# Kernel tuning notes

Measured on AMD Instinct MI355X. Metric: run time of the kernel, lower is better.

## Reference

```python
import jax, jax.numpy as jnp
import numpy as np

N = 50000
E = 800000
IN_DIM = 128
HID = 64
HEADS = 4
OUT_DIM = 121
NEG_SLOPE = 0.2
EPS = 1e-16


def setup_inputs() -> dict:
    key = jax.random.key(0)
    ks = jax.random.split(key, 16)
    glorot = lambda k, shape: jax.random.normal(k, shape, jnp.float32) * (2.0 / (shape[0] + shape[-1])) ** 0.5
    HC = HEADS * HID
    return {
        "x": jax.random.normal(ks[0], (N, IN_DIM), jnp.float32),
        "edge_index": jax.random.randint(ks[1], (2, E), 0, N, jnp.int64),
        # conv1: GATConv(IN_DIM -> HID, heads=HEADS, concat)
        "W1": glorot(ks[2], (IN_DIM, HC)),
        "att_src1": glorot(ks[3], (HEADS, HID)),
        "att_dst1": glorot(ks[4], (HEADS, HID)),
        "b1": jnp.zeros((HC,), jnp.float32),
        # conv2: GATConv(HC -> HID, heads=HEADS, concat)
        "W2": glorot(ks[5], (HC, HC)),
        "att_src2": glorot(ks[6], (HEADS, HID)),
        "att_dst2": glorot(ks[7], (HEADS, HID)),
        "b2": jnp.zeros((HC,), jnp.float32),
        # post_mp: Linear(HC, HID) -> Dropout -> Linear(HID, OUT_DIM)
        "Wm1": glorot(ks[8], (HC, HID)),
        "bm1": jnp.zeros((HID,), jnp.float32),
        "Wm2": glorot(ks[9], (HID, OUT_DIM)),
        "bm2": jnp.zeros((OUT_DIM,), jnp.float32),
    }


def gat_conv(x, src, dst, W, att_src, att_dst, b):
    """PyG GATConv (concat=True, add_self_loops already applied to src/dst)."""
    n = x.shape[0]
    h = (x @ W).reshape(n, HEADS, -1)                     # [N, H, C]
    a_s = jnp.einsum("nhc,hc->nh", h, att_src)            # [N, H]
    a_d = jnp.einsum("nhc,hc->nh", h, att_dst)            # [N, H]
    e = jax.nn.leaky_relu(a_s[src] + a_d[dst], NEG_SLOPE)  # [Etot, H]
    # segment softmax over destination nodes
    m = jax.ops.segment_max(e, dst, num_segments=n)       # [N, H]
    ex = jnp.exp(e - m[dst])
    denom = jax.ops.segment_sum(ex, dst, num_segments=n)  # [N, H]
    alpha = ex / (denom[dst] + EPS)                        # [Etot, H]
    out = jax.ops.segment_sum(alpha[:, :, None] * h[src], dst, num_segments=n)  # [N, H, C]
    return out.reshape(n, -1) + b


def reference(x, edge_index, W1, att_src1, att_dst1, b1, W2, att_src2, att_dst2, b2, Wm1, bm1, Wm2, bm2):
    n = x.shape[0]
    loops = jnp.arange(n, dtype=edge_index.dtype)
    src = jnp.concatenate([edge_index[0], loops])
    dst = jnp.concatenate([edge_index[1], loops])
    h = jax.nn.relu(gat_conv(x, src, dst, W1, att_src1, att_dst1, b1))
    h = jax.nn.relu(gat_conv(h, src, dst, W2, att_src2, att_dst2, b2))
    h = h @ Wm1 + bm1
    h = h @ Wm2 + bm2
    return jax.nn.sigmoid(h)
```

## Files before the change

### kernel.cpp

```cpp
#include <hip/hip_runtime.h>
#include <hip/hip_bf16.h>
#include <float.h>

#define HEADS 4
#define HID 64
#define HC 256
#define NEG_SLOPE 0.2f
#define EPS 1e-16f

typedef short bf16x8 __attribute__((ext_vector_type(8)));
typedef float f32x4 __attribute__((ext_vector_type(4)));
typedef unsigned short ushort8 __attribute__((ext_vector_type(8)));

__device__ __forceinline__ float bflo(unsigned u) { return __uint_as_float(u << 16); }
__device__ __forceinline__ float bfhi(unsigned u) { return __uint_as_float(u & 0xffff0000u); }
__device__ __forceinline__ unsigned packbf2(float a, float b) {
  __hip_bfloat16 ha = __float2bfloat16(a), hb = __float2bfloat16(b);
  unsigned short ua = *reinterpret_cast<unsigned short*>(&ha);
  unsigned short ub = *reinterpret_cast<unsigned short*>(&hb);
  return (unsigned)ua | ((unsigned)ub << 16);
}

#define PK 40

__global__ void __launch_bounds__(256) conv_gemm_attn(
    const __hip_bfloat16* __restrict__ A, const __hip_bfloat16* __restrict__ Bt,
    __hip_bfloat16* __restrict__ Cb,
    const float* __restrict__ att_s, const float* __restrict__ att_d,
    float* __restrict__ a_s, float* __restrict__ a_d,
    float* __restrict__ blockmax, int M, int K) {
  __shared__ unsigned short As[2][64 * PK];
  __shared__ unsigned short Bs[2][256 * PK];
  int tid = threadIdx.x;
  int lane = tid & 63, w = tid >> 6;
  int col16 = lane & 15, quad = lane >> 4;
  int row0 = blockIdx.x * 64;
  const unsigned short* Ag = (const unsigned short*)A;
  const unsigned short* Bg = (const unsigned short*)Bt;

  int ar = tid >> 2;
  int ako = (tid & 3) << 3;
  int agr = row0 + ar; if (agr >= M) agr = M - 1;
  const unsigned short* aga = Ag + (size_t)agr * K + ako;

  f32x4 acc[4][4] = {};
  int niter = K >> 5;

  ushort8 pa, pb[4];
  pa = *(const ushort8*)(aga);
#pragma unroll
  for (int p = 0; p < 4; p++) {
    int i2 = tid + (p << 8);
    int br = i2 >> 2, bko = (i2 & 3) << 3;
    pb[p] = *(const ushort8*)(Bg + (size_t)br * K + bko);
  }
  *(ushort8*)(&As[0][ar * PK + ako]) = pa;
#pragma unroll
  for (int p = 0; p < 4; p++) {
    int i2 = tid + (p << 8);
    int br = i2 >> 2, bko = (i2 & 3) << 3;
    *(ushort8*)(&Bs[0][br * PK + bko]) = pb[p];
  }
  __syncthreads();

  for (int it = 0; it < niter; ++it) {
    int cur = it & 1, nxt = cur ^ 1;
    int k1 = (it + 1) << 5;
    if (it + 1 < niter) {
      pa = *(const ushort8*)(aga + k1);
#pragma unroll
      for (int p = 0; p < 4; p++) {
        int i2 = tid + (p << 8);
        int br = i2 >> 2, bko = (i2 & 3) << 3;
        pb[p] = *(const ushort8*)(Bg + (size_t)br * K + k1 + bko);
      }
    }
    bf16x8 a[4], b[4];
#pragma unroll
    for (int i = 0; i < 4; i++)
      a[i] = *(const bf16x8*)(&As[cur][(i * 16 + col16) * PK + quad * 8]);
#pragma unroll
    for (int j = 0; j < 4; j++)
      b[j] = *(const bf16x8*)(&Bs[cur][((w << 6) + j * 16 + col16) * PK + quad * 8]);
#pragma unroll
    for (int i = 0; i < 4; i++)
#pragma unroll
      for (int j = 0; j < 4; j++)
        acc[i][j] = __builtin_amdgcn_mfma_f32_16x16x32_bf16(a[i], b[j], acc[i][j], 0, 0, 0);
    if (it + 1 < niter) {
      *(ushort8*)(&As[nxt][ar * PK + ako]) = pa;
#pragma unroll
      for (int p = 0; p < 4; p++) {
        int i2 = tid + (p << 8);
        int br = i2 >> 2, bko = (i2 & 3) << 3;
        *(ushort8*)(&Bs[nxt][br * PK + bko]) = pb[p];
      }
    }
    __syncthreads();
  }

#pragma unroll
  for (int i = 0; i < 4; i++) {
#pragma unroll
    for (int j = 0; j < 4; j++) {
      int gc = (w << 6) + j * 16 + col16;
      int grb = row0 + i * 16 + quad * 4;
#pragma unroll
      for (int r = 0; r < 4; r++) {
        int gr = grb + r;
        if (gr < M) Cb[(size_t)gr * 256 + gc] = __float2bfloat16(acc[i][j][r]);
      }
    }
  }

  float ws4[4], wd4[4];
#pragma unroll
  for (int j = 0; j < 4; j++) {
    ws4[j] = att_s[(w << 6) + j * 16 + col16];
    wd4[j] = att_d[(w << 6) + j * 16 + col16];
  }
  float wavemax = -FLT_MAX;
#pragma unroll
  for (int i = 0; i < 4; i++) {
#pragma unroll
    for (int r = 0; r < 4; r++) {
      float vs = 0.f, vd = 0.f;
#pragma unroll
      for (int j = 0; j < 4; j++) {
        vs += acc[i][j][r] * ws4[j];
        vd += acc[i][j][r] * wd4[j];
      }
#pragma unroll
      for (int off = 1; off < 16; off <<= 1) {
        vs += __shfl_xor(vs, off);
        vd += __shfl_xor(vd, off);
      }
      int gr = row0 + i * 16 + quad * 4 + r;
      if (col16 == 0 && gr < M) {
        a_s[(size_t)gr * 4 + w] = vs;
        a_d[(size_t)gr * 4 + w] = vd;
      }
      wavemax = fmaxf(wavemax, vs);
    }
  }
  wavemax = fmaxf(wavemax, __shfl_xor(wavemax, 16));
  wavemax = fmaxf(wavemax, __shfl_xor(wavemax, 32));
  if (lane == 0) blockmax[(size_t)blockIdx.x * 4 + w] = wavemax;
}

__global__ void __launch_bounds__(256) reduce_gmax(const float* __restrict__ blockmax,
                                                   float* __restrict__ gmaxf, int goff, int nb) {
  __shared__ float wm[4][4];
  int tid = threadIdx.x, lane = tid & 63, w = tid >> 6;
  int hd = tid & 3;
  float m = -FLT_MAX;
  for (int i = tid >> 2; i < nb; i += 64)
    m = fmaxf(m, blockmax[(size_t)i * 4 + hd]);
#pragma unroll
  for (int off = 4; off < 64; off <<= 1)
    m = fmaxf(m, __shfl_xor(m, off));
  if (lane < 4) wm[w][lane] = m;
  __syncthreads();
  if (tid < 4) {
    float r = fmaxf(fmaxf(wm[0][tid], wm[1][tid]), fmaxf(wm[2][tid], wm[3][tid]));
    gmaxf[goff + tid] = r;
  }
}

#define TS 72

__global__ void __launch_bounds__(256) postmp_fused(
    const __hip_bfloat16* __restrict__ A, const __hip_bfloat16* __restrict__ Wm1t,
    const __hip_bfloat16* __restrict__ Wm2t, const float* __restrict__ bm1,
    const float* __restrict__ bm2, float* __restrict__ out, int M) {
  __shared__ unsigned short As[128 * PK];
  __shared__ unsigned short Bs[64 * PK];
  __shared__ unsigned short T[128 * TS];
  __shared__ unsigned short W2s[128 * TS];
  int tid = threadIdx.x;
  int lane = tid & 63, w = tid >> 6;
  int col16 = lane & 15, quad = lane >> 4;
  int row0 = blockIdx.x * 128;
  const unsigned short* Ag = (const unsigned short*)A;
  const unsigned short* Bg = (const unsigned short*)Wm1t;
  const unsigned short* W2g = (const unsigned short*)Wm2t;

#pragma unroll
  for (int c = tid; c < 1024; c += 256) {
    int r = c >> 3, ko = (c & 7) << 3;
    ushort8 v = {};
    if (r < 121) v = *(const ushort8*)(W2g + (size_t)r * 64 + ko);
    *(ushort8*)(&W2s[r * TS + ko]) = v;
  }

  f32x4 acc1[2][4] = {};
  for (int k0 = 0; k0 < 256; k0 += 32) {
#pragma unroll
    for (int c = tid; c < 512; c += 256) {
      int r = c >> 2, ko = (c & 3) << 3;
      int gr = row0 + r;
      if (gr >= M) gr = M - 1;
      ushort8 v = *(const ushort8*)(Ag + (size_t)gr * 256 + k0 + ko);
      *(ushort8*)(&As[r * PK + ko]) = v;
    }
    {
      int r = tid >> 2, ko = (tid & 3) << 3;
      ushort8 v = *(const ushort8*)(Bg + (size_t)r * 256 + k0 + ko);
      *(ushort8*)(&Bs[r * PK + ko]) = v;
    }
    __syncthreads();
    bf16x8 a[2], b[4];
#pragma unroll
    for (int i = 0; i < 2; i++)
      a[i] = *(const bf16x8*)(&As[(w * 32 + i * 16 + col16) * PK + quad * 8]);
#pragma unroll
    for (int j = 0; j < 4; j++)
      b[j] = *(const bf16x8*)(&Bs[(j * 16 + col16) * PK + quad * 8]);
#pragma unroll
    for (int i = 0; i < 2; i++)
#pragma unroll
      for (int j = 0; j < 4; j++)
        acc1[i][j] = __builtin_amdgcn_mfma_f32_16x16x32_bf16(a[i], b[j], acc1[i][j], 0, 0, 0);
    __syncthreads();
  }
#pragma unroll
  for (int i = 0; i < 2; i++) {
#pragma unroll
    for (int j = 0; j < 4; j++) {
      int col = j * 16 + col16;
      float bv = bm1[col];
#pragma unroll
      for (int r = 0; r < 4; r++) {
        int rl = w * 32 + i * 16 + quad * 4 + r;
        __hip_bfloat16 hv = __float2bfloat16(acc1[i][j][r] + bv);
        T[rl * TS + col] = *reinterpret_cast<unsigned short*>(&hv);
      }
    }
  }
  __syncthreads();

  int wm2 = w & 1, wn2 = w >> 1;
  f32x4 acc2[4][4] = {};
#pragma unroll
  for (int kk = 0; kk < 2; kk++) {
    bf16x8 a[4], b[4];
#pragma unroll
    for (int i = 0; i < 4; i++)
      a[i] = *(const bf16x8*)(&T[(wm2 * 64 + i * 16 + col16) * TS + kk * 32 + quad * 8]);
#pragma unroll
    for (int j = 0; j < 4; j++)
      b[j] = *(const bf16x8*)(&W2s[(wn2 * 64 + j * 16 + col16) * TS + kk * 32 + quad * 8]);
#pragma unroll
    for (int i = 0; i < 4; i++)
#pragma unroll
      for (int j = 0; j < 4; j++)
        acc2[i][j] = __builtin_amdgcn_mfma_f32_16x16x32_bf16(a[i], b[j], acc2[i][j], 0, 0, 0);
  }
#pragma unroll
  for (int i = 0; i < 4; i++) {
#pragma unroll
    for (int j = 0; j < 4; j++) {
      int gc = wn2 * 64 + j * 16 + col16;
      if (gc >= 121) continue;
      float bv = bm2[gc];
      int grb = row0 + wm2 * 64 + i * 16 + quad * 4;
#pragma unroll
      for (int r = 0; r < 4; r++) {
        int gr = grb + r;
        if (gr >= M) continue;
        float v = acc2[i][j][r] + bv;
        out[(size_t)gr * 121 + gc] = 1.f / (1.f + __expf(-v));
      }
    }
  }
}

__global__ void cast_bf16(const float* __restrict__ src, __hip_bfloat16* __restrict__ dst, int count4) {
  int i = blockIdx.x * 256 + threadIdx.x;
  if (i >= count4) return;
  float4 v = *(const float4*)(src + 4 * (size_t)i);
  uint2 pk;
  pk.x = packbf2(v.x, v.y);
  pk.y = packbf2(v.z, v.w);
  *(uint2*)((unsigned*)dst + 2 * (size_t)i) = pk;
}

__global__ void prep_weights(const float* __restrict__ W1, const float* __restrict__ W2,
                             const float* __restrict__ Wm1, const float* __restrict__ Wm2,
                             __hip_bfloat16* __restrict__ W1t, __hip_bfloat16* __restrict__ W2t,
                             __hip_bfloat16* __restrict__ Wm1t, __hip_bfloat16* __restrict__ Wm2t) {
  int i = blockIdx.x * 256 + threadIdx.x;
  if (i < 128 * 256) {
    int nn = i / 128, kk = i - nn * 128;
    W1t[i] = __float2bfloat16(W1[(size_t)kk * 256 + nn]);
    return;
  }
  i -= 128 * 256;
  if (i < 256 * 256) {
    int nn = i / 256, kk = i - nn * 256;
    W2t[i] = __float2bfloat16(W2[(size_t)kk * 256 + nn]);
    return;
  }
  i -= 256 * 256;
  if (i < 256 * 64) {
    int nn = i / 256, kk = i - nn * 256;
    Wm1t[i] = __float2bfloat16(Wm1[(size_t)kk * 64 + nn]);
    return;
  }
  i -= 256 * 64;
  if (i < 64 * 121) {
    int nn = i / 64, kk = i - nn * 64;
    Wm2t[i] = __float2bfloat16(Wm2[(size_t)kk * 121 + nn]);
  }
}

__global__ void deg_init(int* __restrict__ deg, int n) {
  int i = blockIdx.x * 256 + threadIdx.x;
  if (i < n) deg[i] = 1;
}

__global__ void deg_count(const int* __restrict__ ei, int E, int* __restrict__ deg) {
  int i = blockIdx.x * 256 + threadIdx.x;
  if (i < E) atomicAdd(&deg[ei[E + i]], 1);
}

__global__ void __launch_bounds__(256) scan_block(const int* __restrict__ deg,
                                                  int* __restrict__ row_start,
                                                  int* __restrict__ bsum, int n) {
  __shared__ int wt[4];
  int tid = threadIdx.x, lane = tid & 63, w = tid >> 6;
  int i = blockIdx.x * 256 + tid;
  int v = (i < n) ? deg[i] : 0;
  int s = v;
#pragma unroll
  for (int off = 1; off < 64; off <<= 1) {
    int t = __shfl_up(s, off);
    if (lane >= off) s += t;
  }
  if (lane == 63) wt[w] = s;
  __syncthreads();
  int add = 0;
  if (w > 0) add += wt[0];
  if (w > 1) add += wt[1];
  if (w > 2) add += wt[2];
  if (i < n) row_start[i + 1] = s + add;
  if (tid == 0) bsum[blockIdx.x] = wt[0] + wt[1] + wt[2] + wt[3];
}

__global__ void __launch_bounds__(256) scan_partials(int* __restrict__ bsum, int nb) {
  __shared__ int wt[4];
  int tid = threadIdx.x, lane = tid & 63, w = tid >> 6;
  int v = (tid < nb) ? bsum[tid] : 0;
  int s = v;
#pragma unroll
  for (int off = 1; off < 64; off <<= 1) {
    int t = __shfl_up(s, off);
    if (lane >= off) s += t;
  }
  if (lane == 63) wt[w] = s;
  __syncthreads();
  int add = 0;
  if (w > 0) add += wt[0];
  if (w > 1) add += wt[1];
  if (w > 2) add += wt[2];
  if (tid < nb) bsum[tid] = s + add - v;
}

__global__ void finalize_row(int* __restrict__ row_start, const int* __restrict__ bsum_ex,
                             const int* __restrict__ deg, int* __restrict__ cur, int n) {
  int i = blockIdx.x * 256 + threadIdx.x;
  if (i == 0) row_start[0] = 0;
  if (i < n) {
    int v = row_start[i + 1] + bsum_ex[blockIdx.x];
    row_start[i + 1] = v;
    cur[i] = v - deg[i];
  }
}

__global__ void csr_fill(const int* __restrict__ ei, int E, int n,
                         int* __restrict__ cur, int* __restrict__ csr_src) {
  int i = blockIdx.x * 256 + threadIdx.x;
  int Etot = E + n;
  if (i >= Etot) return;
  int s, d;
  if (i < E) { s = ei[i]; d = ei[E + i]; }
  else { s = d = i - E; }
  int pos = atomicAdd(&cur[d], 1);
  csr_src[pos] = s;
}

__global__ void __launch_bounds__(256) gat_aggregate(
    const __hip_bfloat16* __restrict__ hb, const float* __restrict__ a_src,
    const float* __restrict__ a_dst, const int* __restrict__ row_start,
    const int* __restrict__ csr_src, const float* __restrict__ bias,
    const float* __restrict__ gmaxf, int goff,
    __hip_bfloat16* __restrict__ out, int n) {
  __shared__ float plds[4][256];
  int wid = threadIdx.x >> 6;
  int lane = threadIdx.x & 63;
  int qh = lane >> 4;
  int node = (blockIdx.x << 2) + wid;
  if (node >= n) return;
  float4 adv = *(const float4*)(a_dst + (size_t)node * 4);
  float m0 = gmaxf[goff + 0] + adv.x; m0 = fmaxf(m0, NEG_SLOPE * m0);
  float m1 = gmaxf[goff + 1] + adv.y; m1 = fmaxf(m1, NEG_SLOPE * m1);
  float m2 = gmaxf[goff + 2] + adv.z; m2 = fmaxf(m2, NEG_SLOPE * m2);
  float m3 = gmaxf[goff + 3] + adv.w; m3 = fmaxf(m3, NEG_SLOPE * m3);
  int beg = __builtin_amdgcn_readfirstlane(row_start[node]);
  int end = __builtin_amdgcn_readfirstlane(row_start[node + 1]);
  const unsigned* hw = (const unsigned*)hb;

  float lq = 0.f, cq0 = 0.f, cq1 = 0.f, cq2 = 0.f, cq3 = 0.f;

  for (int cbeg = beg; cbeg < end; cbeg += 64) {
    int cnt = end - cbeg; if (cnt > 64) cnt = 64;
    int eidx = cbeg + (lane < cnt ? lane : cnt - 1);
    int s_l = csr_src[eidx];
    float4 as = *(const float4*)(a_src + (size_t)s_l * 4);
    float v0 = as.x + adv.x; v0 = fmaxf(v0, NEG_SLOPE * v0);
    float v1 = as.y + adv.y; v1 = fmaxf(v1, NEG_SLOPE * v1);
    float v2 = as.z + adv.z; v2 = fmaxf(v2, NEG_SLOPE * v2);
    float v3 = as.w + adv.w; v3 = fmaxf(v3, NEG_SLOPE * v3);
    float p0 = __expf(v0 - m0), p1 = __expf(v1 - m1);
    float p2 = __expf(v2 - m2), p3 = __expf(v3 - m3);
    *(float4*)&plds[wid][lane * 4] = make_float4(p0, p1, p2, p3);
    __builtin_amdgcn_s_waitcnt(0);

    auto step = [&](int jj) {
      int sj = __builtin_amdgcn_readlane(s_l, jj);
      float pq = plds[wid][jj * 4 + qh];
      uint2 d = *(const uint2*)(hw + (size_t)sj * 128 + 2 * lane);
      cq0 += pq * bflo(d.x); cq1 += pq * bfhi(d.x);
      cq2 += pq * bflo(d.y); cq3 += pq * bfhi(d.y);
      lq += pq;
    };
    int j = 0;
    for (; j + 4 <= cnt; j += 4) { step(j); step(j + 1); step(j + 2); step(j + 3); }
    for (; j < cnt; ++j) step(j);
  }

  float4 bq = *(const float4*)(bias + 4 * lane);
  float rq = 1.f / (lq + EPS);
  float o0 = fmaxf(cq0 * rq + bq.x, 0.f);
  float o1 = fmaxf(cq1 * rq + bq.y, 0.f);
  float o2 = fmaxf(cq2 * rq + bq.z, 0.f);
  float o3 = fmaxf(cq3 * rq + bq.w, 0.f);
  uint2 pk;
  pk.x = packbf2(o0, o1);
  pk.y = packbf2(o2, o3);
  *(uint2*)((unsigned*)out + (size_t)node * 128 + 2 * lane) = pk;
}

extern "C" void kernel_launch(void* const* d_in, const int* in_sizes, int n_in,
                              void* d_out, int out_size, void* d_ws, size_t ws_size,
                              hipStream_t stream) {
  const float* x      = (const float*)d_in[0];
  const int*   ei     = (const int*)d_in[1];
  const float* W1     = (const float*)d_in[2];
  const float* att_s1 = (const float*)d_in[3];
  const float* att_d1 = (const float*)d_in[4];
  const float* b1     = (const float*)d_in[5];
  const float* W2     = (const float*)d_in[6];
  const float* att_s2 = (const float*)d_in[7];
  const float* att_d2 = (const float*)d_in[8];
  const float* b2     = (const float*)d_in[9];
  const float* Wm1    = (const float*)d_in[10];
  const float* bm1    = (const float*)d_in[11];
  const float* Wm2    = (const float*)d_in[12];
  const float* bm2    = (const float*)d_in[13];
  float* out = (float*)d_out;

  int n = in_sizes[0] / 128;
  int E = in_sizes[1] / 2;
  int Etot = E + n;

  char* ws = (char*)d_ws;
  size_t off = 0;
  auto carve = [&](size_t bytes) {
    char* p = ws + off;
    off += (bytes + 255) & ~(size_t)255;
    return p;
  };
  __hip_bfloat16* hb   = (__hip_bfloat16*)carve((size_t)n * HC * 2);
  __hip_bfloat16* aggb = (__hip_bfloat16*)carve((size_t)n * HC * 2);
  __hip_bfloat16* xb   = (__hip_bfloat16*)carve((size_t)n * 128 * 2);
  __hip_bfloat16* W1t  = (__hip_bfloat16*)carve((size_t)128 * HC * 2);
  __hip_bfloat16* W2t  = (__hip_bfloat16*)carve((size_t)HC * HC * 2);
  __hip_bfloat16* Wm1t = (__hip_bfloat16*)carve((size_t)HC * HID * 2);
  __hip_bfloat16* Wm2t = (__hip_bfloat16*)carve((size_t)HID * 121 * 2);
  float* as   = (float*)carve((size_t)n * HEADS * 4);
  float* ad   = (float*)carve((size_t)n * HEADS * 4);
  int*   deg  = (int*)carve((size_t)n * 4);
  int*   row  = (int*)carve((size_t)(n + 1) * 4);
  int*   cur  = (int*)carve((size_t)n * 4);
  int*   csr  = (int*)carve((size_t)Etot * 4);
  int*   bsum = (int*)carve((size_t)1024 * 4);
  float* blockmax = (float*)carve((size_t)((n + 63) / 64) * 4 * 4);
  float* gmaxf    = (float*)carve((size_t)8 * 4);
  (void)ws_size;

  int nb256 = (n + 255) / 256;
  int rows64 = (n + 63) / 64;

  cast_bf16<<<(n * 32 + 255) / 256, 256, 0, stream>>>(x, xb, n * 32);
  prep_weights<<<(122432 + 255) / 256, 256, 0, stream>>>(W1, W2, Wm1, Wm2, W1t, W2t, Wm1t, Wm2t);

  deg_init<<<nb256, 256, 0, stream>>>(deg, n);
  deg_count<<<(E + 255) / 256, 256, 0, stream>>>(ei, E, deg);
  scan_block<<<nb256, 256, 0, stream>>>(deg, row, bsum, n);
  scan_partials<<<1, 256, 0, stream>>>(bsum, nb256);
  finalize_row<<<nb256, 256, 0, stream>>>(row, bsum, deg, cur, n);
  csr_fill<<<(Etot + 255) / 256, 256, 0, stream>>>(ei, E, n, cur, csr);

  conv_gemm_attn<<<rows64, 256, 0, stream>>>(
      xb, W1t, hb, att_s1, att_d1, as, ad, blockmax, n, 128);
  reduce_gmax<<<1, 256, 0, stream>>>(blockmax, gmaxf, 0, rows64);
  gat_aggregate<<<(n + 3) / 4, 256, 0, stream>>>(hb, as, ad, row, csr, b1, gmaxf, 0, aggb, n);

  conv_gemm_attn<<<rows64, 256, 0, stream>>>(
      aggb, W2t, hb, att_s2, att_d2, as, ad, blockmax, n, 256);
  reduce_gmax<<<1, 256, 0, stream>>>(blockmax, gmaxf, 4, rows64);
  gat_aggregate<<<(n + 3) / 4, 256, 0, stream>>>(hb, as, ad, row, csr, b2, gmaxf, 4, aggb, n);

  postmp_fused<<<(n + 127) / 128, 256, 0, stream>>>(aggb, Wm1t, Wm2t, bm1, bm2, out, n);
}
```

Baseline: 407.7 us.

## Double-buffer post-MP GEMM loads and process two edges per wave in aggregation

In the post-MP fused kernel, the first GEMM now uses a double-buffered shared-memory layout. The next K-slice is fetched into registers while MFMAs run on the current slice, which removes one barrier per iteration. Shared memory is merged into a single aliased array, and T reuses the A buffer. In gat_aggregate, each half-wave handles a different edge with 16-byte loads (8 bf16 per lane), so each step gathers two source rows, and the halves are combined with a cross-half shuffle at the end. The cost is more registers and some wasted work on padded odd edges.

New measurement: 404.6 us. No clear change (-0.8%).

```diff
diff --git a/kernel.cpp b/kernel.cpp
--- a/kernel.cpp
+++ b/kernel.cpp
@@ -173,10 +173,8 @@
     const __hip_bfloat16* __restrict__ A, const __hip_bfloat16* __restrict__ Wm1t,
     const __hip_bfloat16* __restrict__ Wm2t, const float* __restrict__ bm1,
     const float* __restrict__ bm2, float* __restrict__ out, int M) {
-  __shared__ unsigned short As[128 * PK];
-  __shared__ unsigned short Bs[64 * PK];
-  __shared__ unsigned short T[128 * TS];
-  __shared__ unsigned short W2s[128 * TS];
+  __shared__ unsigned short smem[24576];
+  unsigned short* W2s = &smem[15360];
   int tid = threadIdx.x;
   int lane = tid & 63, w = tid >> 6;
   int col16 = lane & 15, quad = lane >> 4;
@@ -193,36 +191,57 @@
     *(ushort8*)(&W2s[r * TS + ko]) = v;
   }
 
+  int ar0 = tid >> 2, ako = (tid & 3) << 3;
+  int agr0 = row0 + ar0;       if (agr0 >= M) agr0 = M - 1;
+  int agr1 = row0 + ar0 + 64;  if (agr1 >= M) agr1 = M - 1;
+  const unsigned short* aga0 = Ag + (size_t)agr0 * 256 + ako;
+  const unsigned short* aga1 = Ag + (size_t)agr1 * 256 + ako;
+  int br = tid >> 2, bko = (tid & 3) << 3;
+  const unsigned short* bga = Bg + (size_t)br * 256 + bko;
+
   f32x4 acc1[2][4] = {};
-  for (int k0 = 0; k0 < 256; k0 += 32) {
-#pragma unroll
-    for (int c = tid; c < 512; c += 256) {
-      int r = c >> 2, ko = (c & 3) << 3;
-      int gr = row0 + r;
-      if (gr >= M) gr = M - 1;
-      ushort8 v = *(const ushort8*)(Ag + (size_t)gr * 256 + k0 + ko);
-      *(ushort8*)(&As[r * PK + ko]) = v;
-    }
-    {
-      int r = tid >> 2, ko = (tid & 3) << 3;
-      ushort8 v = *(const ushort8*)(Bg + (size_t)r * 256 + k0 + ko);
-      *(ushort8*)(&Bs[r * PK + ko]) = v;
-    }
-    __syncthreads();
+  ushort8 pa0, pa1, pbv;
+  pa0 = *(const ushort8*)(aga0);
+  pa1 = *(const ushort8*)(aga1);
+  pbv = *(const ushort8*)(bga);
+  *(ushort8*)(&smem[ar0 * PK + ako]) = pa0;
+  *(ushort8*)(&smem[(ar0 + 64) * PK + ako]) = pa1;
+  *(ushort8*)(&smem[10240 + br * PK + bko]) = pbv;
+  __syncthreads();
+
+  for (int it = 0; it < 8; ++it) {
+    int cur = it & 1, nxt = cur ^ 1;
+    unsigned short* Asc = &smem[cur * 5120];
+    unsigned short* Bsc = &smem[10240 + cur * 2560];
+    int k1 = (it + 1) << 5;
+    if (it + 1 < 8) {
+      pa0 = *(const ushort8*)(aga0 + k1);
+      pa1 = *(const ushort8*)(aga1 + k1);
+      pbv = *(const ushort8*)(bga + k1);
+    }
     bf16x8 a[2], b[4];
 #pragma unroll
     for (int i = 0; i < 2; i++)
-      a[i] = *(const bf16x8*)(&As[(w * 32 + i * 16 + col16) * PK + quad * 8]);
+      a[i] = *(const bf16x8*)(&Asc[(w * 32 + i * 16 + col16) * PK + quad * 8]);
 #pragma unroll
     for (int j = 0; j < 4; j++)
-      b[j] = *(const bf16x8*)(&Bs[(j * 16 + col16) * PK + quad * 8]);
+      b[j] = *(const bf16x8*)(&Bsc[(j * 16 + col16) * PK + quad * 8]);
 #pragma unroll
     for (int i = 0; i < 2; i++)
 #pragma unroll
       for (int j = 0; j < 4; j++)
         acc1[i][j] = __builtin_amdgcn_mfma_f32_16x16x32_bf16(a[i], b[j], acc1[i][j], 0, 0, 0);
+    if (it + 1 < 8) {
+      unsigned short* Asn = &smem[nxt * 5120];
+      unsigned short* Bsn = &smem[10240 + nxt * 2560];
+      *(ushort8*)(&Asn[ar0 * PK + ako]) = pa0;
+      *(ushort8*)(&Asn[(ar0 + 64) * PK + ako]) = pa1;
+      *(ushort8*)(&Bsn[br * PK + bko]) = pbv;
+    }
     __syncthreads();
   }
+
+  unsigned short* T = &smem[0];
 #pragma unroll
   for (int i = 0; i < 2; i++) {
 #pragma unroll
@@ -398,7 +417,9 @@
   __shared__ float plds[4][256];
   int wid = threadIdx.x >> 6;
   int lane = threadIdx.x & 63;
-  int qh = lane >> 4;
+  int half = lane >> 5;
+  int l32 = lane & 31;
+  int qh = l32 >> 3;
   int node = (blockIdx.x << 2) + wid;
   if (node >= n) return;
   float4 adv = *(const float4*)(a_dst + (size_t)node * 4);
@@ -408,9 +429,11 @@
   float m3 = gmaxf[goff + 3] + adv.w; m3 = fmaxf(m3, NEG_SLOPE * m3);
   int beg = __builtin_amdgcn_readfirstlane(row_start[node]);
   int end = __builtin_amdgcn_readfirstlane(row_start[node + 1]);
-  const unsigned* hw = (const unsigned*)hb;
-
-  float lq = 0.f, cq0 = 0.f, cq1 = 0.f, cq2 = 0.f, cq3 = 0.f;
+  const uint4* hw4 = (const uint4*)hb;
+
+  float lq = 0.f;
+  float c0 = 0.f, c1 = 0.f, c2 = 0.f, c3 = 0.f;
+  float c4 = 0.f, c5 = 0.f, c6 = 0.f, c7 = 0.f;
 
   for (int cbeg = beg; cbeg < end; cbeg += 64) {
     int cnt = end - cbeg; if (cnt > 64) cnt = 64;
@@ -426,29 +449,50 @@
     *(float4*)&plds[wid][lane * 4] = make_float4(p0, p1, p2, p3);
     __builtin_amdgcn_s_waitcnt(0);
 
-    auto step = [&](int jj) {
-      int sj = __builtin_amdgcn_readlane(s_l, jj);
-      float pq = plds[wid][jj * 4 + qh];
-      uint2 d = *(const uint2*)(hw + (size_t)sj * 128 + 2 * lane);
-      cq0 += pq * bflo(d.x); cq1 += pq * bfhi(d.x);
-      cq2 += pq * bflo(d.y); cq3 += pq * bfhi(d.y);
+    auto step = [&](int j) {
+      int jj = j + half;
+      bool dup = jj >= cnt;
+      int jc = dup ? cnt - 1 : jj;
+      int sj = __shfl(s_l, jc);
+      float pq = plds[wid][jc * 4 + qh];
+      if (dup) pq = 0.f;
+      uint4 d = hw4[(size_t)sj * 32 + l32];
+      c0 += pq * bflo(d.x); c1 += pq * bfhi(d.x);
+      c2 += pq * bflo(d.y); c3 += pq * bfhi(d.y);
+      c4 += pq * bflo(d.z); c5 += pq * bfhi(d.z);
+      c6 += pq * bflo(d.w); c7 += pq * bfhi(d.w);
       lq += pq;
     };
     int j = 0;
-    for (; j + 4 <= cnt; j += 4) { step(j); step(j + 1); step(j + 2); step(j + 3); }
-    for (; j < cnt; ++j) step(j);
-  }
-
-  float4 bq = *(const float4*)(bias + 4 * lane);
-  float rq = 1.f / (lq + EPS);
-  float o0 = fmaxf(cq0 * rq + bq.x, 0.f);
-  float o1 = fmaxf(cq1 * rq + bq.y, 0.f);
-  float o2 = fmaxf(cq2 * rq + bq.z, 0.f);
-  float o3 = fmaxf(cq3 * rq + bq.w, 0.f);
-  uint2 pk;
-  pk.x = packbf2(o0, o1);
-  pk.y = packbf2(o2, o3);
-  *(uint2*)((unsigned*)out + (size_t)node * 128 + 2 * lane) = pk;
+    for (; j + 8 <= cnt; j += 8) { step(j); step(j + 2); step(j + 4); step(j + 6); }
+    for (; j < cnt; j += 2) step(j);
+  }
+
+  lq += __shfl_xor(lq, 32);
+  c0 += __shfl_xor(c0, 32); c1 += __shfl_xor(c1, 32);
+  c2 += __shfl_xor(c2, 32); c3 += __shfl_xor(c3, 32);
+  c4 += __shfl_xor(c4, 32); c5 += __shfl_xor(c5, 32);
+  c6 += __shfl_xor(c6, 32); c7 += __shfl_xor(c7, 32);
+
+  if (half == 0) {
+    float4 bA = *(const float4*)(bias + 8 * l32);
+    float4 bB = *(const float4*)(bias + 8 * l32 + 4);
+    float rq = 1.f / (lq + EPS);
+    float o0 = fmaxf(c0 * rq + bA.x, 0.f);
+    float o1 = fmaxf(c1 * rq + bA.y, 0.f);
+    float o2 = fmaxf(c2 * rq + bA.z, 0.f);
+    float o3 = fmaxf(c3 * rq + bA.w, 0.f);
+    float o4 = fmaxf(c4 * rq + bB.x, 0.f);
+    float o5 = fmaxf(c5 * rq + bB.y, 0.f);
+    float o6 = fmaxf(c6 * rq + bB.z, 0.f);
+    float o7 = fmaxf(c7 * rq + bB.w, 0.f);
+    uint4 pk;
+    pk.x = packbf2(o0, o1);
+    pk.y = packbf2(o2, o3);
+    pk.z = packbf2(o4, o5);
+    pk.w = packbf2(o6, o7);
+    *(uint4*)((unsigned*)out + (size_t)node * 128 + l32 * 4) = pk;
+  }
 }
 
 extern "C" void kernel_launch(void* const* d_in, const int* in_sizes, int n_in,
```
